# Performance work log

Measured on AMD Instinct MI355X. Metric: run time of the kernel, lower is better.

The kernel has to match this reference:

```python
import jax, jax.numpy as jnp
import numpy as np

DIM = 1024
HEADS = 16
DIM_HEAD = 64
INNER = HEADS * DIM_HEAD  # 1024
SCALE = DIM_HEAD ** -0.5


def setup_inputs() -> dict:
    key = jax.random.key(0)
    ks = jax.random.split(key, 5)
    B, N = 4, 2048
    x = jax.random.normal(ks[0], (B, N, DIM), dtype=jnp.float32)
    # torch Linear weights are [out, in]; store transposed [in, out] for x @ W
    s = 1.0 / np.sqrt(DIM)
    Wq = jax.random.uniform(ks[1], (DIM, INNER), minval=-s, maxval=s, dtype=jnp.float32)
    Wkv = jax.random.uniform(ks[2], (DIM, 2 * INNER), minval=-s, maxval=s, dtype=jnp.float32)
    so = 1.0 / np.sqrt(INNER)
    Wo = jax.random.uniform(ks[3], (INNER, DIM), minval=-so, maxval=so, dtype=jnp.float32)
    bo = jax.random.uniform(ks[4], (DIM,), minval=-so, maxval=so, dtype=jnp.float32)
    return {"x": x, "Wq": Wq, "Wkv": Wkv, "Wo": Wo, "bo": bo}


def reference(x, Wq, Wkv, Wo, bo):
    B, N, _ = x.shape
    q = x @ Wq                      # [B, N, INNER]
    kv = x @ Wkv                    # [B, N, 2*INNER]
    k, v = jnp.split(kv, 2, axis=-1)

    def split_heads(t):
        return t.reshape(B, N, HEADS, DIM_HEAD).transpose(0, 2, 1, 3)  # [B,H,N,D]

    q, k, v = split_heads(q) * SCALE, split_heads(k), split_heads(v)
    sim = jnp.einsum('bhid,bhjd->bhij', q, k)  # [B,H,N,N]
    mask_value = -jnp.finfo(sim.dtype).max
    # causal: mask strictly-upper triangle (triu with offset j-i+1 = 1)
    causal_mask = jnp.triu(jnp.ones((N, N), dtype=bool), k=1)
    sim = jnp.where(causal_mask[None, None, :, :], mask_value, sim)
    attn = jax.nn.softmax(sim, axis=-1)
    out = jnp.einsum('bhij,bhjd->bhid', attn, v)            # [B,H,N,D]
    out = out.transpose(0, 2, 1, 3).reshape(B, N, INNER)    # [B,N,INNER]
    return out @ Wo + bo
```

## Files before the change

kernel.cpp:

```cpp
#include <hip/hip_runtime.h>

typedef unsigned short u16;
typedef __bf16 bf16x8 __attribute__((ext_vector_type(8)));
typedef float floatx4 __attribute__((ext_vector_type(4)));
typedef unsigned as1_u32 __attribute__((address_space(1)));
typedef unsigned as3_u32 __attribute__((address_space(3)));

__device__ inline u16 f2bf(float f) {
    unsigned int u = __builtin_bit_cast(unsigned int, f);
    u += 0x7fffu + ((u >> 16) & 1u);
    return (u16)(u >> 16);
}
__device__ inline floatx4 mfma16(bf16x8 a, bf16x8 b, floatx4 c) {
    return __builtin_amdgcn_mfma_f32_16x16x32_bf16(a, b, c, 0, 0, 0);
}
__device__ inline void gld16(const u16* g, u16* l) {
    __builtin_amdgcn_global_load_lds((const as1_u32*)g, (as3_u32*)l, 16, 0, 0);
}
__device__ inline unsigned permpack(float lo, float hi) {
    return __builtin_amdgcn_perm(__builtin_bit_cast(unsigned, hi),
                                 __builtin_bit_cast(unsigned, lo), 0x07060302u);
}

#define NSEQ 2048
#define DIM  1024
#define HEADS 16
#define DHEAD 64
#define QSCALE 0.18033688f
#define CSHIFT 4.328085f

__device__ inline void transpose_tile(const float* __restrict__ src,
                                      u16* __restrict__ dst, int ncols,
                                      int n0, int k0, int t) {
    __shared__ u16 tile[64][72];
    #pragma unroll
    for (int rr = 0; rr < 4; rr++) {
        const int k = (t >> 4) + rr * 16;
        const int n = (t & 15) * 4;
        float4 v = *(const float4*)&src[(size_t)(k0 + k) * ncols + n0 + n];
        tile[n + 0][k] = f2bf(v.x); tile[n + 1][k] = f2bf(v.y);
        tile[n + 2][k] = f2bf(v.z); tile[n + 3][k] = f2bf(v.w);
    }
    __syncthreads();
    #pragma unroll
    for (int ww = 0; ww < 2; ww++) {
        const int idx = t + ww * 256;
        const int n = idx >> 3, g = idx & 7;
        u16 tmp[8] __attribute__((aligned(16)));
        #pragma unroll
        for (int i = 0; i < 8; i++) tmp[i] = tile[n][g * 8 + i];
        *(uint4*)&dst[(size_t)(n0 + n) * 1024 + k0 + g * 8] = *(const uint4*)tmp;
    }
}

__global__ __launch_bounds__(256) void prep_fused(
    const float* __restrict__ x,  u16* __restrict__ xb,
    const float* __restrict__ Wq, const float* __restrict__ Wkv,
    u16* __restrict__ Wt)
{
    const int bid = blockIdx.x;
    const int t = threadIdx.x;
    if (bid < 4096) {
        const size_t i = ((size_t)bid * 256 + t) * 8;
        float4 a = *(const float4*)&x[i];
        float4 b = *(const float4*)&x[i + 4];
        u16 o[8] __attribute__((aligned(16)));
        o[0] = f2bf(a.x); o[1] = f2bf(a.y); o[2] = f2bf(a.z); o[3] = f2bf(a.w);
        o[4] = f2bf(b.x); o[5] = f2bf(b.y); o[6] = f2bf(b.z); o[7] = f2bf(b.w);
        *(uint4*)&xb[i] = *(const uint4*)o;
    } else if (bid < 4352) {
        const int v = bid - 4096;
        transpose_tile(Wq, Wt, 1024, (v & 15) * 64, (v >> 4) * 64, t);
    } else {
        const int v = bid - 4352;
        transpose_tile(Wkv, Wt + (size_t)1024 * 1024, 2048, (v & 31) * 64, (v >> 5) * 64, t);
    }
}

__global__ __launch_bounds__(256) void transpose_conv(const float* __restrict__ src,
                                                      u16* __restrict__ dst, int ncols) {
    transpose_tile(src, dst, ncols, blockIdx.x * 64, blockIdx.y * 64, threadIdx.x);
}

__global__ __launch_bounds__(256) void qkv_gemm_v3s(
    const u16* __restrict__ xb, const u16* __restrict__ Wt,
    u16* __restrict__ q_ws, u16* __restrict__ k_ws, u16* __restrict__ v_ws)
{
    __shared__ u16 a0[128 * 32], a1[128 * 32];
    __shared__ u16 b0[128 * 32], b1[128 * 32];

    const int n0 = blockIdx.x * 128;
    const int m0 = blockIdx.y * 128;
    const int t = threadIdx.x, lane = t & 63, w = t >> 6;
    const int wr = w >> 1, wc = w & 1;
    const int quad = lane >> 4, l16 = lane & 15;
    const int lrow = lane >> 2;
    const int lk = (((lane & 3) ^ ((lane >> 3) & 3)) * 8);
    const int rsw = ((l16 >> 1) & 3);

    floatx4 acc[4][4];
    #pragma unroll
    for (int i = 0; i < 4; i++)
        #pragma unroll
        for (int j = 0; j < 4; j++) acc[i][j] = floatx4{0.f, 0.f, 0.f, 0.f};

    for (int k0 = 0; k0 < DIM; k0 += 64) {
        __syncthreads();
        #pragma unroll
        for (int hh = 0; hh < 2; hh++) {
            const int row = w * 32 + hh * 16;
            const size_t ga = (size_t)(m0 + row + lrow) * DIM + k0 + lk;
            const size_t gb = (size_t)(n0 + row + lrow) * DIM + k0 + lk;
            gld16(&xb[ga],      &a0[row * 32]);
            gld16(&xb[ga + 32], &a1[row * 32]);
            gld16(&Wt[gb],      &b0[row * 32]);
            gld16(&Wt[gb + 32], &b1[row * 32]);
        }
        __syncthreads();

        #pragma unroll
        for (int ks = 0; ks < 2; ks++) {
            const u16* al = ks ? a1 : a0;
            const u16* bl = ks ? b1 : b0;
            bf16x8 af[4], bf[4];
            #pragma unroll
            for (int i = 0; i < 4; i++)
                af[i] = *(const bf16x8*)&al[(wr * 64 + i * 16 + l16) * 32
                                            + ((quad ^ rsw) * 8)];
            #pragma unroll
            for (int j = 0; j < 4; j++)
                bf[j] = *(const bf16x8*)&bl[(wc * 64 + j * 16 + l16) * 32
                                            + ((quad ^ rsw) * 8)];
            #pragma unroll
            for (int i = 0; i < 4; i++)
                #pragma unroll
                for (int j = 0; j < 4; j++)
                    acc[i][j] = mfma16(af[i], bf[j], acc[i][j]);
        }
    }

    const int seg = n0 >> 10;
    #pragma unroll
    for (int j = 0; j < 4; j++) {
        const int n  = n0 + wc * 64 + j * 16 + l16;
        const int nn = n & 1023;
        const int h  = nn >> 6, d = nn & 63;
        #pragma unroll
        for (int i = 0; i < 4; i++) {
            const int mb = m0 + wr * 64 + i * 16 + quad * 4;
            const int b = mb >> 11, ib = mb & (NSEQ - 1);
            if (seg == 0) {
                #pragma unroll
                for (int r = 0; r < 4; r++)
                    q_ws[(((size_t)(b * HEADS + h)) * NSEQ + ib + r) * DHEAD + d] =
                        f2bf(acc[i][j][r] * QSCALE);
            } else if (seg == 1) {
                #pragma unroll
                for (int r = 0; r < 4; r++)
                    k_ws[(((size_t)(b * HEADS + h)) * NSEQ + ib + r) * DHEAD + d] =
                        f2bf(acc[i][j][r]);
            } else {
                u16 tmp[4] __attribute__((aligned(8)));
                #pragma unroll
                for (int r = 0; r < 4; r++) tmp[r] = f2bf(acc[i][j][r]);
                *(uint2*)&v_ws[(((size_t)(b * HEADS + h)) * DHEAD + d) * NSEQ + ib] =
                    *(const uint2*)tmp;
            }
        }
    }
}

__global__ __launch_bounds__(256) void attn_v8(
    const u16* __restrict__ q_ws, const u16* __restrict__ k_ws,
    const u16* __restrict__ v_ws, u16* __restrict__ attn_ws)
{
    __shared__ u16 kds[2][64 * 64];
    __shared__ u16 vds[2][64 * 64];
    __shared__ u16 p_lds[4 * 2048];

    const int bid = blockIdx.x;
    const int bh  = bid & 63;
    const int t16 = 15 - (bid >> 6);
    const int i0  = t16 * 128;
    const int b   = bh >> 4, h = bh & 15;

    const u16* qb = q_ws + (size_t)bh * NSEQ * DHEAD;
    const u16* kb = k_ws + (size_t)bh * NSEQ * DHEAD;
    const u16* vb = v_ws + (size_t)bh * DHEAD * NSEQ;

    const int t    = threadIdx.x;
    const int lane = t & 63, w = t >> 6;
    const int quad = lane >> 4, l16 = lane & 15;

    const int srow8 = lane >> 3;
    const int chunk = (lane & 7) ^ srow8;
    const int krow  = w * 16 + srow8;
    const size_t koff = (size_t)krow * DHEAD + chunk * 8;
    const size_t voff = (size_t)krow * NSEQ + chunk * 8;
    u16* klbase = (u16*)&kds[0][0] + w * 1024;
    u16* vlbase = (u16*)&vds[0][0] + w * 1024;
    const int sw = (l16 & 7);

    bf16x8 qf[2][2];
    #pragma unroll
    for (int rf = 0; rf < 2; rf++)
        #pragma unroll
        for (int dg = 0; dg < 2; dg++)
            qf[rf][dg] = *(const bf16x8*)&qb[(size_t)(i0 + rf * 64 + w * 16 + l16) * DHEAD
                                             + dg * 32 + quad * 8];

    floatx4 l4[2] = {floatx4{0.f,0.f,0.f,0.f}, floatx4{0.f,0.f,0.f,0.f}};
    floatx4 acc[2][4];
    #pragma unroll
    for (int rf = 0; rf < 2; rf++)
        #pragma unroll
        for (int dg = 0; dg < 4; dg++) acc[rf][dg] = floatx4{0.f, 0.f, 0.f, 0.f};

    const int jt_max = 2 * t16 + 1;

    gld16(&kb[koff],             klbase);
    gld16(&kb[koff + 8 * DHEAD], klbase + 512);
    gld16(&vb[voff],             vlbase);
    gld16(&vb[voff + 8 * NSEQ],  vlbase + 512);

    for (int jt = 0; jt <= jt_max; jt++) {
        const int cur = jt & 1;
        __syncthreads();

        if (jt < jt_max) {
            const size_t j64 = (size_t)(jt + 1) * 64;
            const int nb = (cur ^ 1) * 4096;
            gld16(&kb[j64 * DHEAD + koff],             klbase + nb);
            gld16(&kb[j64 * DHEAD + koff + 8 * DHEAD], klbase + nb + 512);
            gld16(&vb[j64 + voff],                     vlbase + nb);
            gld16(&vb[j64 + voff + 8 * NSEQ],          vlbase + nb + 512);
        }

        const u16* kl = &kds[cur][0];
        const u16* vl = &vds[cur][0];
        const int j0 = jt * 64;

        floatx4 s[2][4];
        #pragma unroll
        for (int rf = 0; rf < 2; rf++)
            #pragma unroll
            for (int g = 0; g < 4; g++)
                s[rf][g] = floatx4{-CSHIFT, -CSHIFT, -CSHIFT, -CSHIFT};
        __builtin_amdgcn_s_setprio(1);
        #pragma unroll
        for (int dg = 0; dg < 2; dg++)
            #pragma unroll
            for (int g = 0; g < 4; g++) {
                bf16x8 kf = *(const bf16x8*)&kl[(g * 16 + l16) * 64
                                                + (((dg * 4 + quad) ^ sw) * 8)];
                s[0][g] = mfma16(kf, qf[0][dg], s[0][g]);
                s[1][g] = mfma16(kf, qf[1][dg], s[1][g]);
            }
        __builtin_amdgcn_s_setprio(0);

        #pragma unroll
        for (int rf = 0; rf < 2; rf++) {
            const int imin = i0 + rf * 64 + w * 16;
            if (j0 + 63 > imin) {
                const int i = imin + l16;
                #pragma unroll
                for (int g = 0; g < 4; g++) {
                    const int jb = j0 + g * 16 + quad * 4;
                    #pragma unroll
                    for (int r = 0; r < 4; r++)
                        if (jb + r > i) s[rf][g][r] = -1e30f;
                }
            }
        }

        #pragma unroll
        for (int rf = 0; rf < 2; rf++) {
            #pragma unroll
            for (int g = 0; g < 4; g++) {
                #pragma unroll
                for (int r = 0; r < 4; r++)
                    s[rf][g][r] = __builtin_amdgcn_exp2f(s[rf][g][r]);
                l4[rf] += s[rf][g];
                uint2 pk;
                pk.x = permpack(s[rf][g][0], s[rf][g][1]);
                pk.y = permpack(s[rf][g][2], s[rf][g][3]);
                const int c = 2 * g + (quad >> 1);
                *(uint2*)&p_lds[w * 2048 + rf * 1024 + (c >> 2) * 512 + (c & 3) * 128
                                + l16 * 8 + (quad & 1) * 4] = pk;
            }
        }
        asm volatile("s_waitcnt lgkmcnt(0)" ::: "memory");

        __builtin_amdgcn_s_setprio(1);
        #pragma unroll
        for (int jg = 0; jg < 2; jg++) {
            bf16x8 pf0 = *(const bf16x8*)&p_lds[w * 2048 + jg * 512 + quad * 128 + l16 * 8];
            bf16x8 pf1 = *(const bf16x8*)&p_lds[w * 2048 + 1024 + jg * 512 + quad * 128 + l16 * 8];
            #pragma unroll
            for (int dg = 0; dg < 4; dg++) {
                bf16x8 vf = *(const bf16x8*)&vl[(dg * 16 + l16) * 64
                                                + (((jg * 4 + quad) ^ sw) * 8)];
                acc[0][dg] = mfma16(pf0, vf, acc[0][dg]);
                acc[1][dg] = mfma16(pf1, vf, acc[1][dg]);
            }
        }
        __builtin_amdgcn_s_setprio(0);
    }

    #pragma unroll
    for (int rf = 0; rf < 2; rf++) {
        float l_ln = (l4[rf][0] + l4[rf][1]) + (l4[rf][2] + l4[rf][3]);
        l_ln += __shfl_xor(l_ln, 16);
        l_ln += __shfl_xor(l_ln, 32);
        float linv[4];
        #pragma unroll
        for (int r = 0; r < 4; r++)
            linv[r] = 1.0f / __shfl(l_ln, quad * 4 + r);
        #pragma unroll
        for (int dg = 0; dg < 4; dg++)
            #pragma unroll
            for (int r = 0; r < 4; r++) {
                const float o = acc[rf][dg][r] * linv[r];
                const int i = i0 + rf * 64 + w * 16 + quad * 4 + r;
                attn_ws[(((size_t)(b * NSEQ + i)) * HEADS + h) * DHEAD + dg * 16 + l16] =
                    f2bf(o);
            }
    }
}

__global__ __launch_bounds__(256) void out_gemm_v3s(
    const u16* __restrict__ attn, const u16* __restrict__ Wot,
    const float* __restrict__ bo, float* __restrict__ out)
{
    __shared__ u16 a0[128 * 32], a1[128 * 32];
    __shared__ u16 b0[128 * 32], b1[128 * 32];

    const int n0 = blockIdx.x * 128;
    const int m0 = blockIdx.y * 128;
    const int t = threadIdx.x, lane = t & 63, w = t >> 6;
    const int wr = w >> 1, wc = w & 1;
    const int quad = lane >> 4, l16 = lane & 15;
    const int lrow = lane >> 2;
    const int lk = (((lane & 3) ^ ((lane >> 3) & 3)) * 8);
    const int rsw = ((l16 >> 1) & 3);

    floatx4 acc[4][4];
    #pragma unroll
    for (int i = 0; i < 4; i++)
        #pragma unroll
        for (int j = 0; j < 4; j++) acc[i][j] = floatx4{0.f, 0.f, 0.f, 0.f};

    for (int k0 = 0; k0 < DIM; k0 += 64) {
        __syncthreads();
        #pragma unroll
        for (int hh = 0; hh < 2; hh++) {
            const int row = w * 32 + hh * 16;
            const size_t ga = (size_t)(m0 + row + lrow) * DIM + k0 + lk;
            const size_t gb = (size_t)(n0 + row + lrow) * DIM + k0 + lk;
            gld16(&attn[ga],      &a0[row * 32]);
            gld16(&attn[ga + 32], &a1[row * 32]);
            gld16(&Wot[gb],       &b0[row * 32]);
            gld16(&Wot[gb + 32],  &b1[row * 32]);
        }
        __syncthreads();

        #pragma unroll
        for (int ks = 0; ks < 2; ks++) {
            const u16* al = ks ? a1 : a0;
            const u16* bl = ks ? b1 : b0;
            bf16x8 af[4], bf[4];
            #pragma unroll
            for (int i = 0; i < 4; i++)
                af[i] = *(const bf16x8*)&al[(wr * 64 + i * 16 + l16) * 32
                                            + ((quad ^ rsw) * 8)];
            #pragma unroll
            for (int j = 0; j < 4; j++)
                bf[j] = *(const bf16x8*)&bl[(wc * 64 + j * 16 + l16) * 32
                                            + ((quad ^ rsw) * 8)];
            #pragma unroll
            for (int i = 0; i < 4; i++)
                #pragma unroll
                for (int j = 0; j < 4; j++)
                    acc[i][j] = mfma16(af[i], bf[j], acc[i][j]);
        }
    }

    #pragma unroll
    for (int j = 0; j < 4; j++) {
        const int n = n0 + wc * 64 + j * 16 + l16;
        const float bias = bo[n];
        #pragma unroll
        for (int i = 0; i < 4; i++) {
            #pragma unroll
            for (int r = 0; r < 4; r++) {
                const int m = m0 + wr * 64 + i * 16 + quad * 4 + r;
                out[(size_t)m * DIM + n] = acc[i][j][r] + bias;
            }
        }
    }
}

extern "C" void kernel_launch(void* const* d_in, const int* in_sizes, int n_in,
                              void* d_out, int out_size, void* d_ws, size_t ws_size,
                              hipStream_t stream) {
    const float* x   = (const float*)d_in[0];
    const float* Wq  = (const float*)d_in[1];
    const float* Wkv = (const float*)d_in[2];
    const float* Wo  = (const float*)d_in[3];
    const float* bo  = (const float*)d_in[4];

    u16* q_ws = (u16*)d_out;
    u16* xb   = (u16*)d_out + (size_t)8388608;

    u16* ws   = (u16*)d_ws;
    u16* k_ws = ws;
    u16* v_ws = ws + (size_t)8388608;
    u16* a_ws = ws + (size_t)16777216;
    u16* Wt   = a_ws;
    u16* Wot  = k_ws;

    prep_fused<<<4864, 256, 0, stream>>>(x, xb, Wq, Wkv, Wt);
    qkv_gemm_v3s<<<dim3(24, 64), 256, 0, stream>>>(xb, Wt, q_ws, k_ws, v_ws);
    attn_v8<<<dim3(1024), 256, 0, stream>>>(q_ws, k_ws, v_ws, a_ws);
    transpose_conv<<<dim3(16, 16), 256, 0, stream>>>(Wo, Wot, 1024);
    out_gemm_v3s<<<dim3(8, 64), 256, 0, stream>>>(a_ws, Wot, bo, (float*)d_out);
}
```

Baseline: 249.4 us.

## Double-buffer LDS tiles in QKV and output GEMMs with async prefetch

Both GEMM kernels now keep two LDS stages and issue global-to-LDS loads for tile k+2 while tile k is being computed. Explicit vmcnt waits and raw barriers replace the two __syncthreads per iteration, so load latency can overlap the MFMA work. The MFMA block also runs at raised wave priority via s_setprio. The cost is twice the LDS per block (64KB), which may lower occupancy, and a hand-tuned vmcnt count that must match the number of loads issued per stage.

```diff
diff --git a/kernel.cpp b/kernel.cpp
--- a/kernel.cpp
+++ b/kernel.cpp
@@ -82,12 +82,12 @@
     transpose_tile(src, dst, ncols, blockIdx.x * 64, blockIdx.y * 64, threadIdx.x);
 }
 
-__global__ __launch_bounds__(256) void qkv_gemm_v3s(
+__global__ __launch_bounds__(256) void qkv_gemm_v6(
     const u16* __restrict__ xb, const u16* __restrict__ Wt,
     u16* __restrict__ q_ws, u16* __restrict__ k_ws, u16* __restrict__ v_ws)
 {
-    __shared__ u16 a0[128 * 32], a1[128 * 32];
-    __shared__ u16 b0[128 * 32], b1[128 * 32];
+    __shared__ u16 As[2][2][128 * 32];
+    __shared__ u16 Bs[2][2][128 * 32];
 
     const int n0 = blockIdx.x * 128;
     const int m0 = blockIdx.y * 128;
@@ -104,24 +104,34 @@
         #pragma unroll
         for (int j = 0; j < 4; j++) acc[i][j] = floatx4{0.f, 0.f, 0.f, 0.f};
 
-    for (int k0 = 0; k0 < DIM; k0 += 64) {
-        __syncthreads();
-        #pragma unroll
-        for (int hh = 0; hh < 2; hh++) {
-            const int row = w * 32 + hh * 16;
-            const size_t ga = (size_t)(m0 + row + lrow) * DIM + k0 + lk;
-            const size_t gb = (size_t)(n0 + row + lrow) * DIM + k0 + lk;
-            gld16(&xb[ga],      &a0[row * 32]);
-            gld16(&xb[ga + 32], &a1[row * 32]);
-            gld16(&Wt[gb],      &b0[row * 32]);
-            gld16(&Wt[gb + 32], &b1[row * 32]);
-        }
-        __syncthreads();
+#define STAGE_V6(kt, buf) do {                                             \
+    const size_t k0s = (size_t)(kt) * 64;                                  \
+    _Pragma("unroll")                                                      \
+    for (int hh = 0; hh < 2; hh++) {                                       \
+        const int row = w * 32 + hh * 16;                                  \
+        const size_t ga = (size_t)(m0 + row + lrow) * DIM + k0s + lk;      \
+        const size_t gb = (size_t)(n0 + row + lrow) * DIM + k0s + lk;      \
+        gld16(&xb[ga],      &As[buf][0][row * 32]);                        \
+        gld16(&xb[ga + 32], &As[buf][1][row * 32]);                        \
+        gld16(&Wt[gb],      &Bs[buf][0][row * 32]);                        \
+        gld16(&Wt[gb + 32], &Bs[buf][1][row * 32]);                        \
+    }                                                                      \
+} while (0)
+
+    STAGE_V6(0, 0);
+    STAGE_V6(1, 1);
+
+    for (int kt = 0; kt < 16; kt++) {
+        const int cur = kt & 1;
+        if (kt < 15) asm volatile("s_waitcnt vmcnt(8)" ::: "memory");
+        else         asm volatile("s_waitcnt vmcnt(0)" ::: "memory");
+        __builtin_amdgcn_s_barrier();
+        __builtin_amdgcn_sched_barrier(0);
 
         #pragma unroll
         for (int ks = 0; ks < 2; ks++) {
-            const u16* al = ks ? a1 : a0;
-            const u16* bl = ks ? b1 : b0;
+            const u16* al = &As[cur][ks][0];
+            const u16* bl = &Bs[cur][ks][0];
             bf16x8 af[4], bf[4];
             #pragma unroll
             for (int i = 0; i < 4; i++)
@@ -131,13 +141,21 @@
             for (int j = 0; j < 4; j++)
                 bf[j] = *(const bf16x8*)&bl[(wc * 64 + j * 16 + l16) * 32
                                             + ((quad ^ rsw) * 8)];
+            __builtin_amdgcn_s_setprio(1);
             #pragma unroll
             for (int i = 0; i < 4; i++)
                 #pragma unroll
                 for (int j = 0; j < 4; j++)
                     acc[i][j] = mfma16(af[i], bf[j], acc[i][j]);
-        }
-    }
+            __builtin_amdgcn_s_setprio(0);
+        }
+
+        __builtin_amdgcn_sched_barrier(0);
+        __builtin_amdgcn_s_barrier();
+        __builtin_amdgcn_sched_barrier(0);
+        if (kt < 14) STAGE_V6(kt + 2, cur);
+    }
+#undef STAGE_V6
 
     const int seg = n0 >> 10;
     #pragma unroll
@@ -328,12 +346,12 @@
     }
 }
 
-__global__ __launch_bounds__(256) void out_gemm_v3s(
+__global__ __launch_bounds__(256) void out_gemm_v6(
     const u16* __restrict__ attn, const u16* __restrict__ Wot,
     const float* __restrict__ bo, float* __restrict__ out)
 {
-    __shared__ u16 a0[128 * 32], a1[128 * 32];
-    __shared__ u16 b0[128 * 32], b1[128 * 32];
+    __shared__ u16 As[2][2][128 * 32];
+    __shared__ u16 Bs[2][2][128 * 32];
 
     const int n0 = blockIdx.x * 128;
     const int m0 = blockIdx.y * 128;
@@ -350,24 +368,34 @@
         #pragma unroll
         for (int j = 0; j < 4; j++) acc[i][j] = floatx4{0.f, 0.f, 0.f, 0.f};
 
-    for (int k0 = 0; k0 < DIM; k0 += 64) {
-        __syncthreads();
-        #pragma unroll
-        for (int hh = 0; hh < 2; hh++) {
-            const int row = w * 32 + hh * 16;
-            const size_t ga = (size_t)(m0 + row + lrow) * DIM + k0 + lk;
-            const size_t gb = (size_t)(n0 + row + lrow) * DIM + k0 + lk;
-            gld16(&attn[ga],      &a0[row * 32]);
-            gld16(&attn[ga + 32], &a1[row * 32]);
-            gld16(&Wot[gb],       &b0[row * 32]);
-            gld16(&Wot[gb + 32],  &b1[row * 32]);
-        }
-        __syncthreads();
+#define STAGE_O6(kt, buf) do {                                             \
+    const size_t k0s = (size_t)(kt) * 64;                                  \
+    _Pragma("unroll")                                                      \
+    for (int hh = 0; hh < 2; hh++) {                                       \
+        const int row = w * 32 + hh * 16;                                  \
+        const size_t ga = (size_t)(m0 + row + lrow) * DIM + k0s + lk;      \
+        const size_t gb = (size_t)(n0 + row + lrow) * DIM + k0s + lk;      \
+        gld16(&attn[ga],      &As[buf][0][row * 32]);                      \
+        gld16(&attn[ga + 32], &As[buf][1][row * 32]);                      \
+        gld16(&Wot[gb],       &Bs[buf][0][row * 32]);                      \
+        gld16(&Wot[gb + 32],  &Bs[buf][1][row * 32]);                      \
+    }                                                                      \
+} while (0)
+
+    STAGE_O6(0, 0);
+    STAGE_O6(1, 1);
+
+    for (int kt = 0; kt < 16; kt++) {
+        const int cur = kt & 1;
+        if (kt < 15) asm volatile("s_waitcnt vmcnt(8)" ::: "memory");
+        else         asm volatile("s_waitcnt vmcnt(0)" ::: "memory");
+        __builtin_amdgcn_s_barrier();
+        __builtin_amdgcn_sched_barrier(0);
 
         #pragma unroll
         for (int ks = 0; ks < 2; ks++) {
-            const u16* al = ks ? a1 : a0;
-            const u16* bl = ks ? b1 : b0;
+            const u16* al = &As[cur][ks][0];
+            const u16* bl = &Bs[cur][ks][0];
             bf16x8 af[4], bf[4];
             #pragma unroll
             for (int i = 0; i < 4; i++)
@@ -377,13 +405,21 @@
             for (int j = 0; j < 4; j++)
                 bf[j] = *(const bf16x8*)&bl[(wc * 64 + j * 16 + l16) * 32
                                             + ((quad ^ rsw) * 8)];
+            __builtin_amdgcn_s_setprio(1);
             #pragma unroll
             for (int i = 0; i < 4; i++)
                 #pragma unroll
                 for (int j = 0; j < 4; j++)
                     acc[i][j] = mfma16(af[i], bf[j], acc[i][j]);
-        }
-    }
+            __builtin_amdgcn_s_setprio(0);
+        }
+
+        __builtin_amdgcn_sched_barrier(0);
+        __builtin_amdgcn_s_barrier();
+        __builtin_amdgcn_sched_barrier(0);
+        if (kt < 14) STAGE_O6(kt + 2, cur);
+    }
+#undef STAGE_O6
 
     #pragma unroll
     for (int j = 0; j < 4; j++) {
@@ -420,8 +456,8 @@
     u16* Wot  = k_ws;
 
     prep_fused<<<4864, 256, 0, stream>>>(x, xb, Wq, Wkv, Wt);
-    qkv_gemm_v3s<<<dim3(24, 64), 256, 0, stream>>>(xb, Wt, q_ws, k_ws, v_ws);
+    qkv_gemm_v6<<<dim3(24, 64), 256, 0, stream>>>(xb, Wt, q_ws, k_ws, v_ws);
     attn_v8<<<dim3(1024), 256, 0, stream>>>(q_ws, k_ws, v_ws, a_ws);
     transpose_conv<<<dim3(16, 16), 256, 0, stream>>>(Wo, Wot, 1024);
-    out_gemm_v3s<<<dim3(8, 64), 256, 0, stream>>>(a_ws, Wot, bo, (float*)d_out);
-}
+    out_gemm_v6<<<dim3(8, 64), 256, 0, stream>>>(a_ws, Wot, bo, (float*)d_out);
+}
```

After: 249.8 us. Within noise of the previous version (+0.2%).
